# Kernel optimization log

Hardware: AMD Instinct MI355X
Metric: run time of the kernel (lower is better)

The kernel has to match this reference:

```python
import jax, jax.numpy as jnp
import numpy as np

MUL = 32            # num_channels == hidden multiplicity
DIMS = (1, 3, 5)    # dims of 0e, 1o, 2e
HID = MUL * sum(DIMS)   # 288
N_NODES = 10000
N_EDGES = 64000
RHID = 64           # radial MLP hidden_dim
SQM = float(np.sqrt(MUL))


def _cg():
    # Real Clebsch-Gordan-like tensors for l<=2, built from an orthonormal
    # basis B of symmetric traceless 3x3 matrices (the l=2 rep). Each tensor
    # is normalized to unit Frobenius norm (wigner-3j convention).
    s2, s3, s5, s6 = map(np.sqrt, (2.0, 3.0, 5.0, 6.0))
    B = np.zeros((5, 3, 3))
    B[0, 0, 1] = B[0, 1, 0] = 1 / s2
    B[1, 1, 2] = B[1, 2, 1] = 1 / s2
    B[2] = np.diag([-1.0, -1.0, 2.0]) / s6
    B[3, 0, 2] = B[3, 2, 0] = 1 / s2
    B[4] = np.diag([1.0, -1.0, 0.0]) / s2
    C = {}
    C[(0, 0, 0)] = np.ones((1, 1, 1))
    C[(0, 1, 1)] = (np.eye(3) / s3)[None]
    C[(1, 0, 1)] = np.transpose(C[(0, 1, 1)], (1, 0, 2))
    C[(0, 2, 2)] = (np.eye(5) / s5)[None]
    C[(2, 0, 2)] = np.transpose(C[(0, 2, 2)], (1, 0, 2))
    C[(1, 1, 0)] = (np.eye(3) / s3)[:, :, None]
    C[(1, 1, 2)] = np.transpose(B, (1, 2, 0)) / s5   # [3,3,5]
    C[(1, 2, 1)] = np.transpose(B, (1, 0, 2)) / s5   # [3,5,3]
    C[(2, 1, 1)] = B / s5                            # [5,3,3]
    C[(2, 2, 0)] = (np.eye(5) / s5)[:, :, None]
    T = np.einsum('aij,bjk,cki->abc', B, B, B)
    C[(2, 2, 2)] = T / np.linalg.norm(T)
    return {k: jnp.asarray(v, jnp.float32) for k, v in C.items()}

CG = _cg()
# All parity/l-allowed uvw paths for hidden (x) hidden -> hidden
PATHS_FULL = [(0,0,0),(0,1,1),(0,2,2),(1,0,1),(1,1,0),(1,1,2),(1,2,1),(2,0,2),(2,1,1),(2,2,0),(2,2,2)]
# order-2 symmetric TP: i<j use uvw, i==j use uvu (as in _build_symmetric_tp_order2)
O2_UVW = [(0,1,1),(0,2,2),(1,2,1)]
O2_UVU = [(0,0,0),(1,1,0),(1,1,2),(2,2,0),(2,2,2)]


def split(x):
    n = x.shape[0]; o = 0; parts = []
    for d in DIMS:
        parts.append(x[:, o:o + MUL * d].reshape(n, MUL, d)); o += MUL * d
    return parts


def merge(parts):
    n = parts[0].shape[0]
    return jnp.concatenate([p.reshape(n, -1) for p in parts], axis=1)


def lin_irreps(parts, W):
    # e3nn o3.Linear: per-irrep multiplicity mixing, fan-in normalized
    return [jnp.einsum('zui,uw->zwi', parts[l], W[l]) / SQM for l in range(3)]


def pairwise_uvw(xp, yp, W):
    # W: [11, MUL, MUL, MUL]
    n = xp[0].shape[0]
    out = [jnp.zeros((n, MUL, d), xp[0].dtype) for d in DIMS]
    for p, (i, j, k) in enumerate(PATHS_FULL):
        out[k] = out[k] + jnp.einsum('zui,zvj,ijk,uvw->zwk', xp[i], yp[j], CG[(i, j, k)], W[p]) / MUL
    return out


def order2_tp(xp, Wuvw, Wuvu):
    n = xp[0].shape[0]
    out = [jnp.zeros((n, MUL, d), xp[0].dtype) for d in DIMS]
    for p, (i, j, k) in enumerate(O2_UVW):
        out[k] = out[k] + jnp.einsum('zui,zvj,ijk,uvw->zwk', xp[i], xp[j], CG[(i, j, k)], Wuvw[p]) / MUL
    for p, (i, j, k) in enumerate(O2_UVU):
        out[k] = out[k] + jnp.einsum('zui,zvj,ijk,uv->zuk', xp[i], xp[j], CG[(i, j, k)], Wuvu[p]) / SQM
    return out


def _forward(node_features, edge_sh, edge_radial_embedding, edge_attr,
             r_w1, r_b1, r_w2, r_b2, r_w3, r_b3, a_w, a_b, emb_w,
             lin_o1, o2_uvw, o2_uvu, o3a_uvw, o3b_uvw, mix_w, comb_w, self_w,
             edge_index):
    src, dst = edge_index[0], edge_index[1]
    n = node_features.shape[0]
    # scalar node embedding
    h = node_features @ emb_w / SQM                              # [N, MUL]
    # radial MLP -> per-edge TP weights (shared_weights=False)
    rin = jnp.concatenate([edge_radial_embedding, edge_attr], axis=-1)
    rf = jax.nn.silu(rin @ r_w1 + r_b1)
    rf = jax.nn.silu(rf @ r_w2 + r_b2)
    rf = rf @ r_w3 + r_b3                                        # [E, RHID]
    tpw = (rf @ a_w + a_b).reshape(-1, 3, MUL, MUL)              # [E, 3 paths, u, w]
    # A-features: (num_channels x 0e) (x) sh -> hidden, uvw per edge
    h_src = h[src]                                               # [E, MUL]
    msgs, off = [], 0
    for l, d in enumerate(DIMS):
        sh_l = edge_sh[:, off:off + d]; off += d
        mixed = jnp.einsum('eu,euw->ew', h_src, tpw[:, l]) / SQM
        msgs.append(mixed[:, :, None] * sh_l[:, None, :] / jnp.sqrt(jnp.asarray(float(d), mixed.dtype)))
    edge_messages = merge(msgs)                                  # [E, HID]
    a_sum = jax.ops.segment_sum(edge_messages, dst, num_segments=n)
    cnt = jax.ops.segment_sum(jnp.ones((dst.shape[0],), edge_messages.dtype), dst, num_segments=n)
    a = a_sum / jnp.maximum(cnt, 1.0)[:, None]                   # scatter-mean
    ap = split(a)
    # B-features: symmetric contractions of order 1, 2, 3
    b1 = lin_irreps(ap, lin_o1)
    b2 = order2_tp(ap, o2_uvw, o2_uvu)
    b3 = pairwise_uvw(pairwise_uvw(ap, ap, o3a_uvw), ap, o3b_uvw)
    msg = None
    for order, b in enumerate((b1, b2, b3)):
        b = lin_irreps(b, mix_w[order])        # channel_mixing
        c = lin_irreps(b, comb_w[order])       # message_combination
        msg = c if msg is None else [m + x for m, x in zip(msg, c)]
    # self connection: scalar input only has a path to the scalar block
    msg[0] = msg[0] + (node_features @ self_w / SQM)[:, :, None]
    return merge(msg)                                            # [N, HID]


def setup_inputs():
    key = jax.random.key(0)
    ks = jax.random.split(key, 20)
    f = jnp.float32
    inp = {}
    inp['node_features'] = jax.random.normal(ks[0], (N_NODES, MUL), f)
    inp['edge_index'] = jax.random.randint(ks[1], (2, N_EDGES), 0, N_NODES)
    inp['edge_sh'] = jax.random.normal(ks[2], (N_EDGES, 9), f)
    inp['edge_radial_embedding'] = jax.random.uniform(ks[3], (N_EDGES, 8), f)
    inp['edge_attr'] = jax.random.normal(ks[4], (N_EDGES, 16), f)
    inp['r_w1'] = jax.random.normal(ks[5], (24, RHID), f) / np.sqrt(24.0)
    inp['r_b1'] = jnp.zeros((RHID,), f)
    inp['r_w2'] = jax.random.normal(ks[6], (RHID, RHID), f) / np.sqrt(float(RHID))
    inp['r_b2'] = jnp.zeros((RHID,), f)
    inp['r_w3'] = jax.random.normal(ks[7], (RHID, RHID), f) / np.sqrt(float(RHID))
    inp['r_b3'] = jnp.zeros((RHID,), f)
    inp['a_w'] = jax.random.normal(ks[8], (RHID, 3 * MUL * MUL), f) / np.sqrt(float(RHID))
    inp['a_b'] = jnp.zeros((3 * MUL * MUL,), f)
    inp['emb_w'] = jax.random.normal(ks[9], (MUL, MUL), f)
    inp['lin_o1'] = jax.random.normal(ks[10], (3, MUL, MUL), f)
    inp['o2_uvw'] = jax.random.normal(ks[11], (3, MUL, MUL, MUL), f)
    inp['o2_uvu'] = jax.random.normal(ks[12], (5, MUL, MUL), f)
    inp['o3a_uvw'] = jax.random.normal(ks[13], (11, MUL, MUL, MUL), f)
    inp['o3b_uvw'] = jax.random.normal(ks[14], (11, MUL, MUL, MUL), f)
    inp['mix_w'] = jax.random.normal(ks[15], (3, 3, MUL, MUL), f)
    inp['comb_w'] = jax.random.normal(ks[16], (3, 3, MUL, MUL), f)
    inp['self_w'] = jax.random.normal(ks[17], (MUL, MUL), f)
    return inp


def reference(node_features, edge_index, edge_sh, edge_radial_embedding, edge_attr,
              r_w1, r_b1, r_w2, r_b2, r_w3, r_b3, a_w, a_b, emb_w,
              lin_o1, o2_uvw, o2_uvu, o3a_uvw, o3b_uvw, mix_w, comb_w, self_w):
    return _forward(node_features, edge_sh, edge_radial_embedding, edge_attr,
                    r_w1, r_b1, r_w2, r_b2, r_w3, r_b3, a_w, a_b, emb_w,
                    lin_o1, o2_uvw, o2_uvu, o3a_uvw, o3b_uvw, mix_w, comb_w, self_w,
                    edge_index)
```

## Files before the change

kernel.cpp:

```cpp
#include <hip/hip_runtime.h>

#define NN 10000
#define NE 64000
#define INV_SQM 0.17677669529663687f
#define INV_MUL 0.03125f

typedef __attribute__((ext_vector_type(8))) short bfrag;
typedef __attribute__((ext_vector_type(4))) float ffrag;

__device__ __forceinline__ short f2bf(float f) {
  unsigned u = __float_as_uint(f);
  unsigned r = (u + 0x7FFFu + ((u >> 16) & 1u)) >> 16;
  return (short)r;
}

constexpr int cIP[11] = {0,0,0,1,1,1,1,2,2,2,2};
constexpr int cJP[11] = {0,1,2,0,1,1,2,0,1,2,2};
constexpr int cKP[11] = {0,1,2,1,0,2,1,2,1,0,2};
constexpr int cKo[11][6] = {
  {0,1,1,1,1,1},{1,2,3,4,4,4},{4,5,6,7,8,9},{9,10,11,12,12,12},
  {12,15,15,15,15,15},{15,17,19,22,24,26},{26,30,34,37,37,37},
  {37,38,39,40,41,42},{42,46,50,53,53,53},{53,58,58,58,58,58},
  {58,62,68,73,79,83}};
constexpr int cDL[3]  = {1,3,5};
constexpr int cOF[3]  = {0,32,128};
constexpr int cNI[83] = {
  0, 0,0,0, 0,0,0,0,0, 0,1,2, 0,1,2,
  0,1,1,2,0,1,2,0,2,0,1,
  1,0,2,0,0,2,1,1,1,2,0,
  0,1,2,3,4,
  0,2,3,4,0,1,2,4,1,2,3,
  0,1,2,3,4,
  0,2,1,3,0,3,1,2,1,4,0,1,2,3,4,0,1,2,3,3,4,1,2,4,3};
constexpr int cNJ[83] = {
  0, 0,1,2, 0,1,2,3,4, 0,0,0, 0,1,2,
  1,0,2,1,0,1,2,2,0,0,1,
  0,2,3,4,0,1,2,4,1,2,3,
  0,0,0,0,0,
  1,0,2,0,0,2,1,1,1,2,0,
  0,1,2,3,4,
  2,0,3,1,3,0,2,1,4,1,0,1,2,3,4,1,0,3,2,4,3,1,4,2,3};
constexpr float cNV[83] = {
  1.0f,
  0.57735027f,0.57735027f,0.57735027f,
  0.44721360f,0.44721360f,0.44721360f,0.44721360f,0.44721360f,
  0.57735027f,0.57735027f,0.57735027f,
  0.57735027f,0.57735027f,0.57735027f,
  0.31622777f,0.31622777f,0.31622777f,0.31622777f,-0.18257419f,-0.18257419f,
  0.36514837f,0.31622777f,0.31622777f,0.31622777f,-0.31622777f,
  0.31622777f,-0.18257419f,0.31622777f,0.31622777f,0.31622777f,0.31622777f,
  -0.18257419f,-0.31622777f,0.31622777f,0.36514837f,0.31622777f,
  0.44721360f,0.44721360f,0.44721360f,0.44721360f,0.44721360f,
  0.31622777f,-0.18257419f,0.31622777f,0.31622777f,0.31622777f,0.31622777f,
  -0.18257419f,-0.31622777f,0.31622777f,0.36514837f,0.31622777f,
  0.44721360f,0.44721360f,0.44721360f,0.44721360f,0.44721360f,
  -0.23904572f,-0.23904572f,0.20702483f,0.20702483f,
  0.20702483f,0.20702483f,0.11952286f,0.11952286f,-0.20702483f,-0.20702483f,
  -0.23904572f,0.11952286f,0.23904572f,0.11952286f,-0.23904572f,
  0.20702483f,0.20702483f,0.11952286f,0.11952286f,0.20702483f,0.20702483f,
  -0.20702483f,-0.23904572f,-0.23904572f,0.20702483f};

__global__ __launch_bounds__(256) void k_embed(const float* __restrict__ nf,
    const float* __restrict__ emb_w, const float* __restrict__ self_w,
    float* __restrict__ h, float* __restrict__ selfc)
{
  __shared__ float We[1024], Wsf[1024];
  int tid = threadIdx.x;
  for (int i = tid; i < 1024; i += 256) { We[i] = emb_w[i]; Wsf[i] = self_w[i]; }
  __syncthreads();
  int z = blockIdx.x * 8 + (tid >> 5);
  int u = tid & 31;
  if (z >= NN) return;
  const float* row = nf + z * 32;
  float ah = 0.f, as = 0.f;
  #pragma unroll 8
  for (int v = 0; v < 32; ++v) {
    float xv = row[v];
    ah += xv * We[(v << 5) + u];
    as += xv * Wsf[(v << 5) + u];
  }
  h[(z << 5) + u]     = ah * INV_SQM;
  selfc[(z << 5) + u] = as * INV_SQM;
}

__global__ __launch_bounds__(256) void k_radial(
    const float* __restrict__ re, const float* __restrict__ ea,
    const float* __restrict__ w1, const float* __restrict__ b1,
    const float* __restrict__ w2, const float* __restrict__ b2,
    const float* __restrict__ w3, const float* __restrict__ b3,
    float* __restrict__ rf)
{
  __shared__ float W1[24 * 64];
  __shared__ float W2[64 * 64];
  __shared__ float W3[64 * 64];
  __shared__ float rin[32][25];
  __shared__ float t1[32][65], t2[32][65];
  int t = threadIdx.x;
  for (int i = t; i < 24 * 64; i += 256) W1[i] = w1[i];
  for (int i = t; i < 4096; i += 256) { W2[i] = w2[i]; W3[i] = w3[i]; }
  int e0 = blockIdx.x * 32;
  for (int idx = t; idx < 768; idx += 256) {
    int el = idx / 24, i = idx - el * 24;
    int e = e0 + el;
    rin[el][i] = (i < 8) ? re[e * 8 + i] : ea[e * 16 + (i - 8)];
  }
  __syncthreads();
  #pragma unroll
  for (int g = 0; g < 8; ++g) {
    int idx = g * 256 + t, el = idx >> 6, o = idx & 63;
    float acc = b1[o];
    #pragma unroll 8
    for (int i = 0; i < 24; ++i) acc += rin[el][i] * W1[i * 64 + o];
    t1[el][o] = acc / (1.f + __expf(-acc));
  }
  __syncthreads();
  #pragma unroll
  for (int g = 0; g < 8; ++g) {
    int idx = g * 256 + t, el = idx >> 6, o = idx & 63;
    float acc = b2[o];
    #pragma unroll 8
    for (int c = 0; c < 64; ++c) acc += t1[el][c] * W2[(c << 6) + o];
    t2[el][o] = acc / (1.f + __expf(-acc));
  }
  __syncthreads();
  #pragma unroll
  for (int g = 0; g < 8; ++g) {
    int idx = g * 256 + t, el = idx >> 6, o = idx & 63;
    float acc = b3[o];
    #pragma unroll 8
    for (int c = 0; c < 64; ++c) acc += t2[el][c] * W3[(c << 6) + o];
    rf[(e0 + el) * 64 + o] = acc;
  }
}

__global__ __launch_bounds__(256) void k_prepb(const float* __restrict__ aw,
    const float* __restrict__ ab, unsigned short* __restrict__ Bthi,
    unsigned short* __restrict__ Btlo)
{
  int n = blockIdx.x;
  int l = n >> 5, w = n & 31;
  for (int k = threadIdx.x; k < 2080; k += 256) {
    float v = (k < 2048) ? aw[(k >> 5) * 3072 + l * 1024 + (k & 31) * 32 + w]
                         : ab[l * 1024 + (k - 2048) * 32 + w];
    unsigned u = __float_as_uint(v);
    float hif = __uint_as_float(u & 0xffff0000u);
    float lo = v - hif;
    Bthi[n * 2080 + k] = (unsigned short)(u >> 16);
    Btlo[n * 2080 + k] = (unsigned short)(__float_as_uint(lo) >> 16);
  }
}

__global__ __launch_bounds__(256) void k_hist(const int* __restrict__ ei,
                                              int* __restrict__ hch)
{
  __shared__ int lh[NN];
  int tid = threadIdx.x;
  for (int i = tid; i < NN; i += 256) lh[i] = 0;
  __syncthreads();
  atomicAdd(&lh[ei[NE + blockIdx.x * 256 + tid]], 1);
  __syncthreads();
  for (int i = tid; i < NN; i += 256) hch[blockIdx.x * NN + i] = lh[i];
}

__global__ __launch_bounds__(256) void k_tot(const int* __restrict__ hch,
                                             int* __restrict__ tot)
{
  int n = blockIdx.x * 256 + threadIdx.x;
  if (n >= NN) return;
  int s = 0;
  for (int c = 0; c < 250; ++c) s += hch[c * NN + n];
  tot[n] = s;
}

__global__ __launch_bounds__(256) void k_scan(const int* __restrict__ tot,
                                              int* __restrict__ off)
{
  __shared__ int part[256];
  int tid = threadIdx.x;
  int base = tid * 40;
  int s = 0;
  for (int i = 0; i < 40; ++i) { int idx = base + i; if (idx < NN) s += tot[idx]; }
  part[tid] = s;
  __syncthreads();
  if (tid == 0) {
    int acc = 0;
    for (int i = 0; i < 256; ++i) { int t = part[i]; part[i] = acc; acc += t; }
  }
  __syncthreads();
  int acc = part[tid];
  for (int i = 0; i < 40; ++i) {
    int idx = base + i;
    if (idx < NN) { off[idx] = acc; acc += tot[idx]; }
  }
  if (tid == 255) off[NN] = NE;
}

__global__ __launch_bounds__(256) void k_base(const int* __restrict__ off,
    const int* __restrict__ hch, int* __restrict__ basec)
{
  int n = blockIdx.x * 256 + threadIdx.x;
  if (n >= NN) return;
  int acc = off[n];
  for (int c = 0; c < 250; ++c) { basec[c * NN + n] = acc; acc += hch[c * NN + n]; }
}

__global__ __launch_bounds__(256) void k_assign(const int* __restrict__ ei,
    const int* __restrict__ basec, int* __restrict__ eord, int* __restrict__ s2n)
{
  __shared__ int lcnt[NN];
  __shared__ int dstl[256];
  int tid = threadIdx.x, c = blockIdx.x;
  for (int i = tid; i < NN; i += 256) lcnt[i] = 0;
  dstl[tid] = ei[NE + c * 256 + tid];
  __syncthreads();
  int wave = tid >> 6, lane = tid & 63;
  for (int b = 0; b < 4; ++b) {
    if (wave == b) {
      int el = b * 64 + lane;
      int d = dstl[el];
      int rank = 0, last = 1;
      for (int j = 0; j < 64; ++j) {
        int dj = dstl[b * 64 + j];
        if (dj == d) { if (j < lane) rank++; else if (j > lane) last = 0; }
      }
      int slot = basec[c * NN + d] + lcnt[d] + rank;
      eord[slot] = c * 256 + el;
      s2n[slot] = d;
      if (last) lcnt[d] += rank + 1;
    }
    __syncthreads();
  }
}

__global__ __launch_bounds__(256, 2) void k_edge_mfma(
    const float* __restrict__ rf, const float* __restrict__ h,
    const int* __restrict__ ei, const float* __restrict__ sh,
    const unsigned short* __restrict__ Bthi, const unsigned short* __restrict__ Btlo,
    const int* __restrict__ eord, const int* __restrict__ s2n,
    const int* __restrict__ off, float* __restrict__ aout)
{
  __shared__ float smem[12800];
  __shared__ float sh_s[128 * 9];
  __shared__ int ge[128], srcl[128], snl[128];
  int tid = threadIdx.x;
  int s0 = blockIdx.x * 128;
  if (tid < 128) {
    int g = eord[s0 + tid];
    ge[tid] = g;
    srcl[tid] = ei[g];
    snl[tid] = s2n[s0 + tid];
  }
  __syncthreads();
  float* rf_s = smem;
  for (int idx = tid; idx < 128 * 64; idx += 256) {
    int e = idx >> 6, c = idx & 63;
    rf_s[e * 65 + c] = rf[ge[e] * 64 + c];
  }
  for (int idx = tid; idx < 128 * 9; idx += 256) {
    int e = idx / 9, i = idx - e * 9;
    sh_s[idx] = sh[ge[e] * 9 + i];
  }
  __syncthreads();

  int lane = tid & 63, wave = tid >> 6;
  int col = lane & 15, quad = lane >> 4;
  int eA = wave * 32 + col;
  int eB = eA + 16;
  const float* hpA = h + srcl[eA] * 32 + quad * 8;
  const float* hpB = h + srcl[eB] * 32 + quad * 8;
  float4 a0 = *(const float4*)hpA, a1 = *(const float4*)(hpA + 4);
  float4 b0 = *(const float4*)hpB, b1 = *(const float4*)(hpB + 4);
  float ha[8] = {a0.x, a0.y, a0.z, a0.w, a1.x, a1.y, a1.z, a1.w};
  float hb[8] = {b0.x, b0.y, b0.z, b0.w, b1.x, b1.y, b1.z, b1.w};

  ffrag acc[2][6] = {};
  const unsigned short* bhib = Bthi + col * 2080 + quad * 8;
  const unsigned short* blob = Btlo + col * 2080 + quad * 8;

  for (int s = 0; s < 65; ++s) {
    float rA = (s < 64) ? rf_s[eA * 65 + s] : 1.0f;
    float rB = (s < 64) ? rf_s[eB * 65 + s] : 1.0f;
    bfrag hA, lA, hB, lB;
    #pragma unroll
    for (int j = 0; j < 8; ++j) {
      float gA = rA * ha[j];
      unsigned uA = __float_as_uint(gA);
      hA[j] = (short)(uA >> 16);
      float loA = gA - __uint_as_float(uA & 0xffff0000u);
      lA[j] = (short)(__float_as_uint(loA) >> 16);
      float gB = rB * hb[j];
      unsigned uB = __float_as_uint(gB);
      hB[j] = (short)(uB >> 16);
      float loB = gB - __uint_as_float(uB & 0xffff0000u);
      lB[j] = (short)(__float_as_uint(loB) >> 16);
    }
    int ko = s << 5;
    #pragma unroll
    for (int t = 0; t < 6; ++t) {
      bfrag bh = *(const bfrag*)(bhib + t * 16 * 2080 + ko);
      bfrag bl = *(const bfrag*)(blob + t * 16 * 2080 + ko);
      acc[0][t] = __builtin_amdgcn_mfma_f32_16x16x32_bf16(hA, bh, acc[0][t], 0, 0, 0);
      acc[1][t] = __builtin_amdgcn_mfma_f32_16x16x32_bf16(hB, bh, acc[1][t], 0, 0, 0);
      acc[0][t] = __builtin_amdgcn_mfma_f32_16x16x32_bf16(lA, bh, acc[0][t], 0, 0, 0);
      acc[1][t] = __builtin_amdgcn_mfma_f32_16x16x32_bf16(lB, bh, acc[1][t], 0, 0, 0);
      acc[0][t] = __builtin_amdgcn_mfma_f32_16x16x32_bf16(hA, bl, acc[0][t], 0, 0, 0);
      acc[1][t] = __builtin_amdgcn_mfma_f32_16x16x32_bf16(hB, bl, acc[1][t], 0, 0, 0);
    }
  }

  __syncthreads();
  float* mix = smem;
  #pragma unroll
  for (int mt = 0; mt < 2; ++mt)
    #pragma unroll
    for (int r = 0; r < 4; ++r) {
      int el = wave * 32 + mt * 16 + quad * 4 + r;
      #pragma unroll
      for (int t = 0; t < 6; ++t) {
        int m = ((t >> 1) << 5) + ((t & 1) << 4) + col;
        mix[el * 100 + m] = acc[mt][t][r] * INV_SQM;
      }
    }
  __syncthreads();

  int m_[2], shi_[2];
  float nrm_[2];
  int ncid = (tid < 32) ? 2 : 1;
  #pragma unroll
  for (int q = 0; q < 2; ++q) {
    int c = q ? 256 + tid : tid;
    int l, w, i;
    if (c < 32) { l = 0; w = c; i = 0; }
    else if (c < 128) { l = 1; w = (c - 32) / 3; i = (c - 32) % 3; }
    else { l = 2; w = (c - 128) / 5; i = (c - 128) % 5; }
    m_[q] = l * 32 + w;
    shi_[q] = (l == 0) ? 0 : ((l == 1) ? 1 + i : 4 + i);
    nrm_[q] = (l == 0) ? 1.0f : ((l == 1) ? 0.57735027f : 0.44721360f);
  }
  int s = 0;
  while (s < 128) {
    int n = snl[s];
    int e2 = s + 1;
    while (e2 < 128 && snl[e2] == n) ++e2;
    int o0 = off[n], o1 = off[n + 1];
    float inv = 1.0f / (float)(o1 - o0);
    bool interior = (o0 == s0 + s) && (o1 == s0 + e2);
    float v[2] = {0.f, 0.f};
    for (int el = s; el < e2; ++el) {
      v[0] += mix[el * 100 + m_[0]] * sh_s[el * 9 + shi_[0]];
      if (ncid == 2) v[1] += mix[el * 100 + m_[1]] * sh_s[el * 9 + shi_[1]];
    }
    #pragma unroll
    for (int q = 0; q < 2; ++q) {
      if (q >= ncid) break;
      float val = v[q] * nrm_[q] * inv;
      int c = q ? 256 + tid : tid;
      if (interior) aout[n * 288 + c] = val;
      else atomicAdd(&aout[n * 288 + c], val);
    }
    s = e2;
  }
}

__global__ __launch_bounds__(256) void k_prepw(const float* __restrict__ W,
                                               unsigned short* __restrict__ Wt)
{
  __shared__ float buf[32 * 33];
  int tid = threadIdx.x;
  long base = (long)blockIdx.x * 1024;
  #pragma unroll
  for (int it = 0; it < 4; ++it) {
    int idx = it * 256 + tid;
    int w = idx & 31, v = idx >> 5;
    buf[w * 33 + v] = W[base + v * 32 + w];
  }
  __syncthreads();
  unsigned* out32 = (unsigned*)(Wt + base);
  #pragma unroll
  for (int it = 0; it < 2; ++it) {
    int idx = it * 256 + tid;
    int w = idx >> 4, vp = idx & 15;
    float f0 = buf[w * 33 + vp * 2], f1 = buf[w * 33 + vp * 2 + 1];
    unsigned pk = (unsigned)(unsigned short)f2bf(f0) |
                  ((unsigned)(unsigned short)f2bf(f1) << 16);
    out32[w * 16 + vp] = pk;
  }
}

template<int PI, int WIDX>
__device__ __forceinline__ void process_path(const float* __restrict__ x_s,
    const float* __restrict__ y_s, const unsigned short* __restrict__ wt,
    int lane, int wave, ffrag acc[9][2])
{
  constexpr int ip = cIP[PI], jp = cJP[PI], kp = cKP[PI];
  constexpr int di = cDL[ip], dj = cDL[jp], dk = cDL[kp];
  constexpr int xb = cOF[ip], yb = cOF[jp];
  constexpr int ks0 = (kp == 0) ? 0 : ((kp == 1) ? 1 : 4);
  constexpr int nA = cKo[PI][0];
  constexpr int nB = cKo[PI][dk];
  const int z = lane & 15, quad = lane >> 4;

  float yreg[8][dj];
  #pragma unroll
  for (int vi = 0; vi < 8; ++vi)
    #pragma unroll
    for (int j = 0; j < dj; ++j)
      yreg[vi][j] = y_s[z * 292 + yb + (quad * 8 + vi) * dj + j];

  for (int uu = 0; uu < 8; ++uu) {
    int u = wave * 8 + uu;
    const unsigned short* wb = wt + (((WIDX * 32 + u) * 32) << 5) + quad * 8;
    bfrag b0 = *(const bfrag*)(wb + (z << 5));
    bfrag b1 = *(const bfrag*)(wb + ((16 + z) << 5));
    float xv[di];
    #pragma unroll
    for (int i = 0; i < di; ++i) xv[i] = x_s[z * 292 + xb + u * di + i];
    float xc[nB - nA];
    #pragma unroll
    for (int n = nA; n < nB; ++n) xc[n - nA] = xv[cNI[n]] * cNV[n];
    bfrag fa[dk];
    #pragma unroll
    for (int vi = 0; vi < 8; ++vi) {
      float T[dk];
      #pragma unroll
      for (int k = 0; k < dk; ++k) T[k] = 0.f;
      #pragma unroll
      for (int k = 0; k < dk; ++k)
        #pragma unroll
        for (int n = cKo[PI][k]; n < cKo[PI][k + 1]; ++n)
          T[k] += xc[n - nA] * yreg[vi][cNJ[n]];
      #pragma unroll
      for (int k = 0; k < dk; ++k) fa[k][vi] = f2bf(T[k]);
    }
    #pragma unroll
    for (int k = 0; k < dk; ++k) {
      acc[ks0 + k][0] = __builtin_amdgcn_mfma_f32_16x16x32_bf16(fa[k], b0, acc[ks0 + k][0], 0, 0, 0);
      acc[ks0 + k][1] = __builtin_amdgcn_mfma_f32_16x16x32_bf16(fa[k], b1, acc[ks0 + k][1], 0, 0, 0);
    }
  }
}

template<int MODE>
__global__ __launch_bounds__(256, 2) void k_pairwise_mfma(
    const float* __restrict__ x, const float* __restrict__ y,
    const unsigned short* __restrict__ wt, float* __restrict__ out, float scale)
{
  __shared__ float smem[9504];
  float* x_s = smem;
  float* y_s = smem + 4672;
  int tid = threadIdx.x;
  int z0 = blockIdx.x * 16;
  for (int idx = tid; idx < 16 * 72; idx += 256) {
    int r = idx / 72, f = (idx - r * 72) * 4;
    *(float4*)&x_s[r * 292 + f] = *(const float4*)&x[(z0 + r) * 288 + f];
    *(float4*)&y_s[r * 292 + f] = *(const float4*)&y[(z0 + r) * 288 + f];
  }
  __syncthreads();
  int lane = tid & 63, wave = tid >> 6;
  ffrag acc[9][2] = {};

  if constexpr (MODE == 0) {
    process_path<0, 0>(x_s, y_s, wt, lane, wave, acc);
    process_path<1, 1>(x_s, y_s, wt, lane, wave, acc);
    process_path<2, 2>(x_s, y_s, wt, lane, wave, acc);
    process_path<3, 3>(x_s, y_s, wt, lane, wave, acc);
    process_path<4, 4>(x_s, y_s, wt, lane, wave, acc);
    process_path<5, 5>(x_s, y_s, wt, lane, wave, acc);
    process_path<6, 6>(x_s, y_s, wt, lane, wave, acc);
    process_path<7, 7>(x_s, y_s, wt, lane, wave, acc);
    process_path<8, 8>(x_s, y_s, wt, lane, wave, acc);
    process_path<9, 9>(x_s, y_s, wt, lane, wave, acc);
    process_path<10, 10>(x_s, y_s, wt, lane, wave, acc);
  } else {
    process_path<1, 0>(x_s, y_s, wt, lane, wave, acc);
    process_path<2, 1>(x_s, y_s, wt, lane, wave, acc);
    process_path<6, 2>(x_s, y_s, wt, lane, wave, acc);
  }

  float* slice0 = smem;
  float* slice1 = smem + 4752;
  int n15 = lane & 15, quad = lane >> 4;
  __syncthreads();
  if (wave >= 2) {
    float* sl = (wave == 2) ? slice0 : slice1;
    #pragma unroll
    for (int s = 0; s < 9; ++s)
      #pragma unroll
      for (int wh = 0; wh < 2; ++wh)
        #pragma unroll
        for (int r = 0; r < 4; ++r)
          sl[(s * 16 + quad * 4 + r) * 33 + wh * 16 + n15] = acc[s][wh][r];
  }
  __syncthreads();
  if (wave < 2) {
    float* sl = (wave == 0) ? slice0 : slice1;
    #pragma unroll
    for (int s = 0; s < 9; ++s)
      #pragma unroll
      for (int wh = 0; wh < 2; ++wh)
        #pragma unroll
        for (int r = 0; r < 4; ++r)
          acc[s][wh][r] += sl[(s * 16 + quad * 4 + r) * 33 + wh * 16 + n15];
  }
  __syncthreads();
  if (wave == 1) {
    #pragma unroll
    for (int s = 0; s < 9; ++s)
      #pragma unroll
      for (int wh = 0; wh < 2; ++wh)
        #pragma unroll
        for (int r = 0; r < 4; ++r)
          slice1[(s * 16 + quad * 4 + r) * 33 + wh * 16 + n15] = acc[s][wh][r];
  }
  __syncthreads();
  if (wave == 0) {
    #pragma unroll
    for (int s = 0; s < 9; ++s)
      #pragma unroll
      for (int wh = 0; wh < 2; ++wh)
        #pragma unroll
        for (int r = 0; r < 4; ++r) {
          int o = (s * 16 + quad * 4 + r) * 33 + wh * 16 + n15;
          slice0[o] = acc[s][wh][r] + slice1[o];
        }
  }
  __syncthreads();
  for (int idx = tid; idx < 4608; idx += 256) {
    int w = idx & 31, rest = idx >> 5;
    int zz = rest & 15, ks = rest >> 4;
    int c = (ks == 0) ? w : (ks < 4 ? 32 + w * 3 + (ks - 1) : 128 + w * 5 + (ks - 4));
    out[(z0 + zz) * 288 + c] = scale * slice0[(ks * 16 + zz) * 33 + w];
  }
}

template<int PI>
__device__ __forceinline__ void uvu_path(const float* __restrict__ x_t,
    const float* __restrict__ Wg, int u, int zq, float acc0[2], float acc2[2][5])
{
  constexpr int ip = cIP[PI], jp = cJP[PI], kp = cKP[PI];
  constexpr int di = cDL[ip], dj = cDL[jp], dk = cDL[kp];
  constexpr int xb = cOF[ip], yb = cOF[jp];
  constexpr int nA = cKo[PI][0];
  constexpr int nB = cKo[PI][dk];
  float wrow[32];
  #pragma unroll
  for (int vq = 0; vq < 8; ++vq)
    *(float4*)&wrow[vq * 4] = *(const float4*)&Wg[u * 32 + vq * 4];
  #pragma unroll
  for (int zz = 0; zz < 2; ++zz) {
    int z = zq + (zz << 3);
    float xv[di];
    #pragma unroll
    for (int i = 0; i < di; ++i) xv[i] = x_t[z * 288 + xb + u * di + i];
    float xc[nB - nA];
    #pragma unroll
    for (int n = nA; n < nB; ++n) xc[n - nA] = xv[cNI[n]] * cNV[n];
    const float* yrb = &x_t[z * 288 + yb];
    #pragma unroll 8
    for (int v = 0; v < 32; ++v) {
      float yv[dj];
      #pragma unroll
      for (int j = 0; j < dj; ++j) yv[j] = yrb[v * dj + j];
      float wv = wrow[v];
      if constexpr (kp == 0) {
        float t = 0.f;
        #pragma unroll
        for (int n = nA; n < nB; ++n) t += xc[n - nA] * yv[cNJ[n]];
        acc0[zz] += wv * t;
      } else {
        #pragma unroll
        for (int k = 0; k < 5; ++k) {
          float t = 0.f;
          #pragma unroll
          for (int n = cKo[PI][k]; n < cKo[PI][k + 1]; ++n)
            t += xc[n - nA] * yv[cNJ[n]];
          acc2[zz][k] += wv * t;
        }
      }
    }
  }
}

__global__ __launch_bounds__(256) void k_uvu(
    const float* __restrict__ x, const float* __restrict__ W, float* __restrict__ out)
{
  __shared__ __align__(16) float x_t[16 * 288];
  int tid = threadIdx.x;
  int z0 = blockIdx.x * 16;
  for (int idx = tid; idx < 16 * 72; idx += 256) {
    int r = idx / 72, f = idx - r * 72;
    *(float4*)&x_t[r * 288 + f * 4] = *(const float4*)&x[(z0 + r) * 288 + f * 4];
  }
  __syncthreads();
  int u = tid & 31, zq = tid >> 5;
  float acc0[2] = {0.f, 0.f};
  float acc2[2][5] = {};
  uvu_path<0>(x_t, W,            u, zq, acc0, acc2);
  uvu_path<4>(x_t, W + 1 * 1024, u, zq, acc0, acc2);
  uvu_path<5>(x_t, W + 2 * 1024, u, zq, acc0, acc2);
  uvu_path<9>(x_t, W + 3 * 1024, u, zq, acc0, acc2);
  uvu_path<10>(x_t, W + 4 * 1024, u, zq, acc0, acc2);
  #pragma unroll
  for (int zz = 0; zz < 2; ++zz) {
    int zg = z0 + zq + (zz << 3);
    float* orow = out + zg * 288;
    orow[u] += INV_SQM * acc0[zz];
    #pragma unroll
    for (int kk = 0; kk < 5; ++kk) orow[128 + u * 5 + kk] += INV_SQM * acc2[zz][kk];
  }
}

__device__ __forceinline__ void lin_row(float* dst, const float* src, const float* Wm, int w)
{
  {
    float s = 0.f;
    for (int u = 0; u < 32; ++u) s += src[u] * Wm[(u << 5) + w];
    dst[w] = s * INV_SQM;
  }
  #pragma unroll
  for (int i = 0; i < 3; ++i) {
    float s = 0.f;
    for (int u = 0; u < 32; ++u) s += src[32 + u * 3 + i] * Wm[1024 + (u << 5) + w];
    dst[32 + w * 3 + i] = s * INV_SQM;
  }
  #pragma unroll
  for (int i = 0; i < 5; ++i) {
    float s = 0.f;
    for (int u = 0; u < 32; ++u) s += src[128 + u * 5 + i] * Wm[2048 + (u << 5) + w];
    dst[128 + w * 5 + i] = s * INV_SQM;
  }
}

__device__ __forceinline__ void lin_acc(float* msg, const float* src, const float* Wm, int w)
{
  {
    float s = 0.f;
    for (int u = 0; u < 32; ++u) s += src[u] * Wm[(u << 5) + w];
    msg[0] += s * INV_SQM;
  }
  #pragma unroll
  for (int i = 0; i < 3; ++i) {
    float s = 0.f;
    for (int u = 0; u < 32; ++u) s += src[32 + u * 3 + i] * Wm[1024 + (u << 5) + w];
    msg[1 + i] += s * INV_SQM;
  }
  #pragma unroll
  for (int i = 0; i < 5; ++i) {
    float s = 0.f;
    for (int u = 0; u < 32; ++u) s += src[128 + u * 5 + i] * Wm[2048 + (u << 5) + w];
    msg[4 + i] += s * INV_SQM;
  }
}

__global__ __launch_bounds__(256) void k_finalize(
    const float* __restrict__ a, const float* __restrict__ b2, const float* __restrict__ b3,
    const float* __restrict__ selfc, const float* __restrict__ lin_o1,
    const float* __restrict__ mix_w, const float* __restrict__ comb_w,
    float* __restrict__ out)
{
  __shared__ float bufA[8 * 288];
  __shared__ float bufB[8 * 288];
  int tid = threadIdx.x;
  int w = tid & 31, zl = tid >> 5;
  int z = blockIdx.x * 8 + zl;
  float msg[9];
  #pragma unroll
  for (int s = 0; s < 9; ++s) msg[s] = 0.f;
  float* rowA = &bufA[zl * 288];
  float* rowB = &bufB[zl * 288];
  lin_row(rowA, a + z * 288, lin_o1, w);
  __syncthreads();
  lin_row(rowB, rowA, mix_w, w);
  __syncthreads();
  lin_acc(msg, rowB, comb_w, w);
  __syncthreads();
  lin_row(rowA, b2 + z * 288, mix_w + 3072, w);
  __syncthreads();
  lin_acc(msg, rowA, comb_w + 3072, w);
  __syncthreads();
  lin_row(rowA, b3 + z * 288, mix_w + 6144, w);
  __syncthreads();
  lin_acc(msg, rowA, comb_w + 6144, w);

  float sc = selfc[(z << 5) + w];
  float* orow = out + z * 288;
  orow[w] = msg[0] + sc;
  #pragma unroll
  for (int i = 0; i < 3; ++i) orow[32 + w * 3 + i] = msg[1 + i];
  #pragma unroll
  for (int i = 0; i < 5; ++i) orow[128 + w * 5 + i] = msg[4 + i];
}

extern "C" void kernel_launch(void* const* d_in, const int* in_sizes, int n_in,
                              void* d_out, int out_size, void* d_ws, size_t ws_size,
                              hipStream_t stream)
{
  (void)in_sizes; (void)n_in; (void)out_size; (void)ws_size;
  const float* nf   = (const float*)d_in[0];
  const int*   ei   = (const int*)d_in[1];
  const float* sh   = (const float*)d_in[2];
  const float* re   = (const float*)d_in[3];
  const float* ea   = (const float*)d_in[4];
  const float* rw1  = (const float*)d_in[5];
  const float* rb1  = (const float*)d_in[6];
  const float* rw2  = (const float*)d_in[7];
  const float* rb2  = (const float*)d_in[8];
  const float* rw3  = (const float*)d_in[9];
  const float* rb3  = (const float*)d_in[10];
  const float* aw   = (const float*)d_in[11];
  const float* ab   = (const float*)d_in[12];
  const float* embw = (const float*)d_in[13];
  const float* lino1= (const float*)d_in[14];
  const float* o2uvw= (const float*)d_in[15];
  const float* o2uvu= (const float*)d_in[16];
  const float* o3a  = (const float*)d_in[17];
  const float* o3b  = (const float*)d_in[18];
  const float* mixw = (const float*)d_in[19];
  const float* combw= (const float*)d_in[20];
  const float* selfw= (const float*)d_in[21];
  float* out = (float*)d_out;
  float* ws  = (float*)d_ws;

  float* h     = ws;
  float* selfc = ws + 320000;
  float* rfb   = ws + 640000;
  float* a     = ws + 4736000;
  int*   tot   = (int*)(ws + 7616000);
  float* cint  = ws + 7626000;
  float* b2 = rfb;
  float* b3 = cint;
  unsigned short* wt_o2  = (unsigned short*)(ws + 10506000);
  unsigned short* wt_o3a = wt_o2 + 98304;
  unsigned short* wt_o3b = wt_o3a + 360448;
  unsigned short* bthi   = (unsigned short*)cint;
  unsigned short* btlo   = bthi + 199680;
  int* h_chunk = (int*)a;
  int* basec   = (int*)(cint + 200000);
  int* eord    = (int*)(cint + 2700000);
  int* s2n     = (int*)(cint + 2764000);
  int* off     = (int*)(cint + 2828000);

  k_prepb<<<96, 256, 0, stream>>>(aw, ab, bthi, btlo);
  k_prepw<<<96, 256, 0, stream>>>(o2uvw, wt_o2);
  k_prepw<<<352, 256, 0, stream>>>(o3a, wt_o3a);
  k_prepw<<<352, 256, 0, stream>>>(o3b, wt_o3b);
  k_embed<<<1250, 256, 0, stream>>>(nf, embw, selfw, h, selfc);
  k_radial<<<2000, 256, 0, stream>>>(re, ea, rw1, rb1, rw2, rb2, rw3, rb3, rfb);
  k_hist<<<250, 256, 0, stream>>>(ei, h_chunk);
  k_tot<<<40, 256, 0, stream>>>(h_chunk, tot);
  k_scan<<<1, 256, 0, stream>>>(tot, off);
  k_base<<<40, 256, 0, stream>>>(off, h_chunk, basec);
  k_assign<<<250, 256, 0, stream>>>(ei, basec, eord, s2n);
  hipMemsetAsync(a, 0, 2880000 * sizeof(float), stream);
  k_edge_mfma<<<500, 256, 0, stream>>>(rfb, h, ei, sh, bthi, btlo, eord, s2n, off, a);
  k_pairwise_mfma<1><<<625, 256, 0, stream>>>(a, a, wt_o2, b2, INV_MUL);
  k_uvu<<<625, 256, 0, stream>>>(a, o2uvu, b2);
  k_pairwise_mfma<0><<<625, 256, 0, stream>>>(a, a, wt_o3a, cint, INV_MUL);
  k_pairwise_mfma<0><<<625, 256, 0, stream>>>(cint, a, wt_o3b, b3, INV_MUL);
  k_finalize<<<1250, 256, 0, stream>>>(a, b2, b3, selfc, lino1, mixw, combw, out);
}
```

Baseline: 961.1 us.

## Precompose finalize linear weights and replace edge atomics with boundary partial fixup

A new prep kernel multiplies lin_o1·mix·comb (and mix·comb for the other branches) into nine combined 32x32 matrices, folding in the normalization scales. Finalize then applies one linear map per branch from shared memory instead of chained lin_row/lin_acc passes with barriers. In the edge kernel, nodes cut by a block boundary now write partials to a buffer instead of using atomicAdd, and a small fixup kernel sums the two halves. The fixup assumes a node spans at most two blocks (degree ≤128), and the workspace regions are reused.

```diff
diff --git a/kernel.cpp b/kernel.cpp
--- a/kernel.cpp
+++ b/kernel.cpp
@@ -237,7 +237,8 @@
     const int* __restrict__ ei, const float* __restrict__ sh,
     const unsigned short* __restrict__ Bthi, const unsigned short* __restrict__ Btlo,
     const int* __restrict__ eord, const int* __restrict__ s2n,
-    const int* __restrict__ off, float* __restrict__ aout)
+    const int* __restrict__ off, float* __restrict__ aout,
+    float* __restrict__ bpart)
 {
   __shared__ float smem[12800];
   __shared__ float sh_s[128 * 9];
@@ -344,7 +345,8 @@
     while (e2 < 128 && snl[e2] == n) ++e2;
     int o0 = off[n], o1 = off[n + 1];
     float inv = 1.0f / (float)(o1 - o0);
-    bool interior = (o0 == s0 + s) && (o1 == s0 + e2);
+    bool headcut = (o0 < s0 + s);
+    bool tailcut = (o1 > s0 + e2);
     float v[2] = {0.f, 0.f};
     for (int el = s; el < e2; ++el) {
       v[0] += mix[el * 100 + m_[0]] * sh_s[el * 9 + shi_[0]];
@@ -355,11 +357,24 @@
       if (q >= ncid) break;
       float val = v[q] * nrm_[q] * inv;
       int c = q ? 256 + tid : tid;
-      if (interior) aout[n * 288 + c] = val;
-      else atomicAdd(&aout[n * 288 + c], val);
+      if (!headcut && !tailcut) aout[n * 288 + c] = val;
+      else bpart[(blockIdx.x * 2 + (headcut ? 0 : 1)) * 288 + c] = val;
     }
     s = e2;
   }
+}
+
+__global__ __launch_bounds__(256) void k_fix(const int* __restrict__ s2n,
+    const int* __restrict__ off, const float* __restrict__ bpart,
+    float* __restrict__ aout)
+{
+  int i = blockIdx.x;
+  int slot = (i + 1) * 128;
+  int n = s2n[slot];
+  if (off[n] == slot) return;
+  for (int c = threadIdx.x; c < 288; c += 256)
+    aout[n * 288 + c] = bpart[(i * 2 + 1) * 288 + c]
+                      + bpart[((i + 1) * 2 + 0) * 288 + c];
 }
 
 __global__ __launch_bounds__(256) void k_prepw(const float* __restrict__ W,
@@ -384,6 +399,43 @@
     unsigned pk = (unsigned)(unsigned short)f2bf(f0) |
                   ((unsigned)(unsigned short)f2bf(f1) << 16);
     out32[w * 16 + vp] = pk;
+  }
+}
+
+__global__ __launch_bounds__(256) void k_prepc(const float* __restrict__ lino1,
+    const float* __restrict__ mixw, const float* __restrict__ combw,
+    float* __restrict__ wc)
+{
+  __shared__ float A[1024], B[1024], T[1024];
+  int o = blockIdx.x / 3, l = blockIdx.x - o * 3;
+  int tid = threadIdx.x;
+  const float* M = mixw + (o * 3 + l) * 1024;
+  const float* C = combw + (o * 3 + l) * 1024;
+  if (o == 0) {
+    for (int i = tid; i < 1024; i += 256) { A[i] = lino1[l * 1024 + i]; B[i] = M[i]; }
+    __syncthreads();
+    #pragma unroll
+    for (int it = 0; it < 4; ++it) {
+      int idx = it * 256 + tid;
+      int u = idx >> 5, w = idx & 31;
+      float s = 0.f;
+      for (int v = 0; v < 32; ++v) s += A[(u << 5) + v] * B[(v << 5) + w];
+      T[idx] = s;
+    }
+  } else {
+    for (int i = tid; i < 1024; i += 256) T[i] = M[i];
+  }
+  __syncthreads();
+  for (int i = tid; i < 1024; i += 256) A[i] = C[i];
+  __syncthreads();
+  float scale = (o == 0) ? INV_SQM * INV_SQM * INV_SQM : INV_SQM * INV_SQM;
+  #pragma unroll
+  for (int it = 0; it < 4; ++it) {
+    int idx = it * 256 + tid;
+    int u = idx >> 5, w = idx & 31;
+    float s = 0.f;
+    for (int v = 0; v < 32; ++v) s += T[(u << 5) + v] * A[(v << 5) + w];
+    wc[(o * 3 + l) * 1024 + idx] = s * scale;
   }
 }
 
@@ -610,78 +662,46 @@
   }
 }
 
-__device__ __forceinline__ void lin_row(float* dst, const float* src, const float* Wm, int w)
-{
-  {
-    float s = 0.f;
-    for (int u = 0; u < 32; ++u) s += src[u] * Wm[(u << 5) + w];
-    dst[w] = s * INV_SQM;
-  }
-  #pragma unroll
-  for (int i = 0; i < 3; ++i) {
-    float s = 0.f;
-    for (int u = 0; u < 32; ++u) s += src[32 + u * 3 + i] * Wm[1024 + (u << 5) + w];
-    dst[32 + w * 3 + i] = s * INV_SQM;
-  }
-  #pragma unroll
-  for (int i = 0; i < 5; ++i) {
-    float s = 0.f;
-    for (int u = 0; u < 32; ++u) s += src[128 + u * 5 + i] * Wm[2048 + (u << 5) + w];
-    dst[128 + w * 5 + i] = s * INV_SQM;
-  }
-}
-
-__device__ __forceinline__ void lin_acc(float* msg, const float* src, const float* Wm, int w)
-{
-  {
-    float s = 0.f;
-    for (int u = 0; u < 32; ++u) s += src[u] * Wm[(u << 5) + w];
-    msg[0] += s * INV_SQM;
-  }
-  #pragma unroll
-  for (int i = 0; i < 3; ++i) {
-    float s = 0.f;
-    for (int u = 0; u < 32; ++u) s += src[32 + u * 3 + i] * Wm[1024 + (u << 5) + w];
-    msg[1 + i] += s * INV_SQM;
-  }
-  #pragma unroll
-  for (int i = 0; i < 5; ++i) {
-    float s = 0.f;
-    for (int u = 0; u < 32; ++u) s += src[128 + u * 5 + i] * Wm[2048 + (u << 5) + w];
-    msg[4 + i] += s * INV_SQM;
-  }
-}
-
 __global__ __launch_bounds__(256) void k_finalize(
-    const float* __restrict__ a, const float* __restrict__ b2, const float* __restrict__ b3,
-    const float* __restrict__ selfc, const float* __restrict__ lin_o1,
-    const float* __restrict__ mix_w, const float* __restrict__ comb_w,
-    float* __restrict__ out)
-{
-  __shared__ float bufA[8 * 288];
-  __shared__ float bufB[8 * 288];
-  int tid = threadIdx.x;
+    const float* __restrict__ a, const float* __restrict__ b2,
+    const float* __restrict__ b3, const float* __restrict__ selfc,
+    const float* __restrict__ wc, float* __restrict__ out)
+{
+  __shared__ float W[9216];
+  __shared__ float S[6912];
+  int tid = threadIdx.x;
+  int z0 = blockIdx.x * 8;
+  for (int i = tid; i < 9216; i += 256) W[i] = wc[i];
+  const float* srcs[3] = {a, b2, b3};
+  for (int o = 0; o < 3; ++o)
+    for (int idx = tid; idx < 8 * 72; idx += 256) {
+      int r = idx / 72, f = (idx - r * 72) * 4;
+      *(float4*)&S[o * 2304 + r * 288 + f] = *(const float4*)&srcs[o][(z0 + r) * 288 + f];
+    }
+  __syncthreads();
   int w = tid & 31, zl = tid >> 5;
-  int z = blockIdx.x * 8 + zl;
   float msg[9];
   #pragma unroll
   for (int s = 0; s < 9; ++s) msg[s] = 0.f;
-  float* rowA = &bufA[zl * 288];
-  float* rowB = &bufB[zl * 288];
-  lin_row(rowA, a + z * 288, lin_o1, w);
-  __syncthreads();
-  lin_row(rowB, rowA, mix_w, w);
-  __syncthreads();
-  lin_acc(msg, rowB, comb_w, w);
-  __syncthreads();
-  lin_row(rowA, b2 + z * 288, mix_w + 3072, w);
-  __syncthreads();
-  lin_acc(msg, rowA, comb_w + 3072, w);
-  __syncthreads();
-  lin_row(rowA, b3 + z * 288, mix_w + 6144, w);
-  __syncthreads();
-  lin_acc(msg, rowA, comb_w + 6144, w);
-
+  #pragma unroll
+  for (int o = 0; o < 3; ++o) {
+    const float* src = &S[o * 2304 + zl * 288];
+    const float* W0 = &W[(o * 3 + 0) * 1024];
+    const float* W1 = &W[(o * 3 + 1) * 1024];
+    const float* W2 = &W[(o * 3 + 2) * 1024];
+    #pragma unroll
+    for (int u = 0; u < 32; ++u) {
+      float w0 = W0[(u << 5) + w];
+      msg[0] += src[u] * w0;
+      float w1 = W1[(u << 5) + w];
+      #pragma unroll
+      for (int i = 0; i < 3; ++i) msg[1 + i] += src[32 + u * 3 + i] * w1;
+      float w2 = W2[(u << 5) + w];
+      #pragma unroll
+      for (int i = 0; i < 5; ++i) msg[4 + i] += src[128 + u * 5 + i] * w2;
+    }
+  }
+  int z = z0 + zl;
   float sc = selfc[(z << 5) + w];
   float* orow = out + z * 288;
   orow[w] = msg[0] + sc;
@@ -726,6 +746,7 @@
   float* rfb   = ws + 640000;
   float* a     = ws + 4736000;
   int*   tot   = (int*)(ws + 7616000);
+  float* wc    = ws + 7616000;
   float* cint  = ws + 7626000;
   float* b2 = rfb;
   float* b3 = cint;
@@ -736,6 +757,7 @@
   unsigned short* btlo   = bthi + 199680;
   int* h_chunk = (int*)a;
   int* basec   = (int*)(cint + 200000);
+  float* bpart = cint + 200000;
   int* eord    = (int*)(cint + 2700000);
   int* s2n     = (int*)(cint + 2764000);
   int* off     = (int*)(cint + 2828000);
@@ -751,11 +773,13 @@
   k_scan<<<1, 256, 0, stream>>>(tot, off);
   k_base<<<40, 256, 0, stream>>>(off, h_chunk, basec);
   k_assign<<<250, 256, 0, stream>>>(ei, basec, eord, s2n);
+  k_prepc<<<9, 256, 0, stream>>>(lino1, mixw, combw, wc);
   hipMemsetAsync(a, 0, 2880000 * sizeof(float), stream);
-  k_edge_mfma<<<500, 256, 0, stream>>>(rfb, h, ei, sh, bthi, btlo, eord, s2n, off, a);
+  k_edge_mfma<<<500, 256, 0, stream>>>(rfb, h, ei, sh, bthi, btlo, eord, s2n, off, a, bpart);
+  k_fix<<<499, 256, 0, stream>>>(s2n, off, bpart, a);
   k_pairwise_mfma<1><<<625, 256, 0, stream>>>(a, a, wt_o2, b2, INV_MUL);
   k_uvu<<<625, 256, 0, stream>>>(a, o2uvu, b2);
   k_pairwise_mfma<0><<<625, 256, 0, stream>>>(a, a, wt_o3a, cint, INV_MUL);
   k_pairwise_mfma<0><<<625, 256, 0, stream>>>(cint, a, wt_o3b, b3, INV_MUL);
-  k_finalize<<<1250, 256, 0, stream>>>(a, b2, b3, selfc, lino1, mixw, combw, out);
-}
+  k_finalize<<<1250, 256, 0, stream>>>(a, b2, b3, selfc, wc, out);
+}
```

New measurement: 811.8 us. -15.5%, faster.
